# Optimization experiments

Hardware: AMD Instinct MI355X
Metric: run time of the kernel (lower is better)

## Reference

```python
import jax, jax.numpy as jnp
import numpy as np

B, N, K = 16, 1024, 20
BOX = 10.0
IN_DIM = 78
HID = 128


def setup_inputs() -> dict:
    key = jax.random.key(0)
    k1, k2, k3, k4, k5 = jax.random.split(key, 5)
    position = jax.random.uniform(k1, (B, N, 3), dtype=jnp.float32) * BOX
    # random proper orthonormal orientation matrices via QR
    R_raw = jax.random.normal(k2, (B, N, 3, 3), dtype=jnp.float32)
    orientation_R, _ = jnp.linalg.qr(R_raw)
    w1 = jax.random.normal(k3, (IN_DIM, HID), jnp.float32) * (1.0 / np.sqrt(IN_DIM))
    b1 = jnp.zeros((HID,), jnp.float32)
    w2 = jax.random.normal(k4, (HID, HID), jnp.float32) * (1.0 / np.sqrt(HID))
    b2 = jnp.zeros((HID,), jnp.float32)
    w3 = jax.random.normal(k5, (HID, 1), jnp.float32) * (1.0 / np.sqrt(HID))
    b3 = jnp.zeros((1,), jnp.float32)
    return dict(position=position, orientation_R=orientation_R,
                w1=w1, b1=b1, w2=w2, b2=b2, w3=w3, b3=b3)


def _features(position, orientation_R):
    # all-pairs displacement with minimum-image periodic boundary
    dr = position[:, :, None, :] - position[:, None, :, :]        # (B,N,N,3)
    dr = dr - BOX * jnp.round(dr / BOX)
    r2 = jnp.sum(dr * dr, axis=-1)                                # (B,N,N)
    r2 = r2 + jnp.eye(N, dtype=r2.dtype) * 1e9                    # exclude self
    neg_r2, idx = jax.lax.top_k(-r2, K)                           # (B,N,K)
    NN_R = jnp.sqrt(-neg_r2)[..., None]                           # (B,N,K,1)
    NN_dr = jnp.take_along_axis(dr, idx[..., None], axis=2)       # (B,N,K,3)
    u = NN_dr / NN_R                                              # unit separation
    inv_r = 1.0 / NN_R
    bidx = jnp.arange(B)[:, None, None]
    Rn = orientation_R[bidx, idx]                                 # (B,N,K,3,3) neighbor frames
    Rp = orientation_R                                            # (B,N,3,3) particle frame
    # pairwise dot products of principal axes: (B,N,K,3,3)
    dot = jnp.einsum('bnij,bnklj->bnkil', Rp, Rn)
    # elementwise products of every axis pair: (B,N,K,3,3,3)
    elem = Rp[:, :, None, :, None, :] * Rn[:, :, :, None, :, :]
    elem_norm = jnp.linalg.norm(elem, axis=-1)                    # (B,N,K,3,3)
    # cross products of corresponding principal axes: (B,N,K,3,3)
    cross = jnp.cross(Rp[:, :, None, :, :], Rn)
    cross_norm = jnp.linalg.norm(cross, axis=-1)                  # (B,N,K,3)
    # relative orientation R_i^T R_j: (B,N,K,3,3)
    rel = jnp.einsum('bnji,bnkjl->bnkil', Rp, Rn)
    # RBF of dr projected on principal axes
    rbf_p = jnp.exp(-jnp.einsum('bnkd,bnid->bnki', u, Rp) ** 2)   # (B,N,K,3)
    rbf_n = jnp.exp(-jnp.einsum('bnkd,bnkid->bnki', u, Rn) ** 2)  # (B,N,K,3)
    tr = rel[..., 0, 0] + rel[..., 1, 1] + rel[..., 2, 2]
    angle = jnp.arccos(jnp.clip((tr - 1.0) * 0.5, -1.0 + 1e-6, 1.0 - 1e-6))[..., None]
    feats = jnp.concatenate([
        NN_R, inv_r, u,
        dot.reshape(B, N, K, 9),
        elem.reshape(B, N, K, 27),
        elem_norm.reshape(B, N, K, 9),
        cross.reshape(B, N, K, 9),
        cross_norm,
        rel.reshape(B, N, K, 9),
        rbf_p, rbf_n, angle,
    ], axis=-1)                                                   # (B,N,K,78)
    return feats


def reference(position, orientation_R, w1, b1, w2, b2, w3, b3):
    f = _features(position, orientation_R)                        # (B,N,K,78)
    h = jnp.tanh(f @ w1 + b1)
    h = jnp.tanh(h @ w2 + b2)
    pooled = jnp.max(h, axis=2)                                   # max-pool over neighbors
    energy = pooled @ w3 + b3                                     # (B,N,1)
    return energy
```

## Files before the change

### kernel.cpp

```cpp
#include <hip/hip_runtime.h>
#include <hip/hip_bf16.h>

namespace {

constexpr int B = 16;
constexpr int N = 1024;
constexpr int K = 20;
constexpr int HID = 128;
constexpr float BOX = 10.0f;

constexpr int PPB = 4;
constexpr int MROWS = PPB * K;
constexpr int MT = 5;
constexpr int KP1 = 96;
constexpr int FP = 104;
constexpr int H1P = 136;
constexpr int SURVCAP = 96;

constexpr uint HBASE = 1872;

typedef __attribute__((ext_vector_type(8))) short short8;
typedef __attribute__((ext_vector_type(4))) float f32x4;

__device__ __forceinline__ float tanh_f(float x) {
    float e = __expf(2.0f * x);
    return 1.0f - 2.0f / (e + 1.0f);
}

__device__ __forceinline__ ushort bfb(float x) {
    __hip_bfloat16 h = __float2bfloat16(x);
    return __builtin_bit_cast(ushort, h);
}

__device__ __forceinline__ uint r2bin(uint key) {
    int bv = (int)(key >> 19) - (int)HBASE;
    return (uint)min(255, max(0, bv));
}

__device__ __forceinline__ float pbc(float d) {
    const float hi = __fsub_rn(d, BOX);
    const float lo = __fadd_rn(d, BOX);
    return d > 5.0f ? hi : (d < -5.0f ? lo : d);
}

__global__ __launch_bounds__(256) void conv_w_kernel(
    const float* __restrict__ w1, const float* __restrict__ w2,
    ushort* __restrict__ w1Th, ushort* __restrict__ w1Tl,
    ushort* __restrict__ w2Th, ushort* __restrict__ w2Tl)
{
    const int idx = blockIdx.x * 256 + threadIdx.x;
    if (idx < 128 * KP1) {
        const int n = idx / KP1, k = idx - n * KP1;
        const float v = (k < 78) ? w1[k * HID + n] : 0.0f;
        const __hip_bfloat16 h = __float2bfloat16(v);
        w1Th[idx] = __builtin_bit_cast(ushort, h);
        w1Tl[idx] = bfb(v - __bfloat162float(h));
    } else if (idx < 128 * KP1 + 128 * 128) {
        const int i = idx - 128 * KP1;
        const int n = i >> 7, k = i & 127;
        const float v = w2[k * HID + n];
        const __hip_bfloat16 h = __float2bfloat16(v);
        w2Th[i] = __builtin_bit_cast(ushort, h);
        w2Tl[i] = bfb(v - __bfloat162float(h));
    }
}

__global__ __launch_bounds__(256, 4) void fused_kernel(
    const float* __restrict__ pos, const float* __restrict__ ori,
    const float* __restrict__ b1, const float* __restrict__ b2,
    const float* __restrict__ w3, const float* __restrict__ b3,
    const ushort* __restrict__ w1Th, const ushort* __restrict__ w1Tl,
    const ushort* __restrict__ w2Th, const ushort* __restrict__ w2Tl,
    float* __restrict__ out)
{
    __shared__ __align__(16) __hip_bfloat16 fS[MROWS][FP];
    __shared__ __align__(16) ushort h1S[MROWS][H1P];
    __shared__ int   nbrS[PPB][K];
    __shared__ float RpS[PPB][9];
    __shared__ float red[4][PPB];
    __shared__ int   TS[PPB];
    __shared__ uint  scntS[PPB];

    uint* const histS = (uint*)&h1S[0][0];
    unsigned long long* const survS =
        (unsigned long long*)((char*)&h1S[0][0] + 4096);

    const int pid0 = blockIdx.x * PPB;
    const int b  = pid0 >> 10;
    const int nb = pid0 & (N - 1);
    const int t  = threadIdx.x;
    const float* posb = pos + (size_t)b * N * 3;
    const float* orib = ori + (size_t)b * N * 9;

#pragma unroll
    for (int i = 0; i < 4; ++i) histS[i * 256 + t] = 0;
    if (t < PPB) scntS[t] = 0;
    if (t < PPB * 9) RpS[t / 9][t % 9] = orib[(size_t)(nb + t / 9) * 9 + (t % 9)];

    float cx[PPB], cy[PPB], cz[PPB];
#pragma unroll
    for (int p = 0; p < PPB; ++p) {
        cx[p] = posb[(nb + p) * 3 + 0];
        cy[p] = posb[(nb + p) * 3 + 1];
        cz[p] = posb[(nb + p) * 3 + 2];
    }

    float r2v[PPB][4];
#pragma unroll
    for (int q = 0; q < 4; ++q) {
        const int j = t + q * 256;
        const float px = posb[j * 3 + 0];
        const float py = posb[j * 3 + 1];
        const float pz = posb[j * 3 + 2];
#pragma unroll
        for (int p = 0; p < PPB; ++p) {
            const float dx = pbc(__fsub_rn(cx[p], px));
            const float dy = pbc(__fsub_rn(cy[p], py));
            const float dz = pbc(__fsub_rn(cz[p], pz));
            float r2 = __fadd_rn(__fadd_rn(__fmul_rn(dx, dx), __fmul_rn(dy, dy)),
                                 __fmul_rn(dz, dz));
            if (j == nb + p) r2 = 1e9f;
            r2v[p][q] = r2;
        }
    }
    __syncthreads();

#pragma unroll
    for (int p = 0; p < PPB; ++p)
#pragma unroll
        for (int q = 0; q < 4; ++q)
            atomicAdd(&histS[p * 256 + r2bin(__float_as_uint(r2v[p][q]))], 1u);
    __syncthreads();

    {
        const int p = t >> 6, lane = t & 63;
        const uint* hp = histS + p * 256;
        const uint h0 = hp[4 * lane + 0], h1v = hp[4 * lane + 1];
        const uint h2v = hp[4 * lane + 2], h3v = hp[4 * lane + 3];
        const uint s = h0 + h1v + h2v + h3v;
        uint inc = s;
#pragma unroll
        for (int off = 1; off < 64; off <<= 1) {
            const uint v = __shfl_up(inc, off, 64);
            if (lane >= off) inc += v;
        }
        const uint exc = inc - s;
        if (exc < (uint)K && inc >= (uint)K) {
            uint c = exc; int Tb = -1;
            c += h0;  if (Tb < 0 && c >= (uint)K) Tb = 4 * lane + 0;
            c += h1v; if (Tb < 0 && c >= (uint)K) Tb = 4 * lane + 1;
            c += h2v; if (Tb < 0 && c >= (uint)K) Tb = 4 * lane + 2;
            c += h3v; if (Tb < 0 && c >= (uint)K) Tb = 4 * lane + 3;
            TS[p] = Tb;
        }
    }
    __syncthreads();

#pragma unroll
    for (int p = 0; p < PPB; ++p) {
        const uint T = (uint)TS[p];
#pragma unroll
        for (int q = 0; q < 4; ++q) {
            const uint key = __float_as_uint(r2v[p][q]);
            if (r2bin(key) <= T) {
                const uint pp = atomicAdd(&scntS[p], 1u);
                if (pp < (uint)SURVCAP)
                    survS[p * SURVCAP + pp] =
                        ((unsigned long long)key << 32) | (uint)(t + q * 256);
            }
        }
    }
    __syncthreads();

    {
        const int p = t >> 6;
        const int S = min((int)scntS[p], SURVCAP);
        const unsigned long long* sp = survS + p * SURVCAP;
#pragma unroll
        for (int half = 0; half < 2; ++half) {
            const int s = (t & 63) + half * 64;
            if (s < S) {
                const unsigned long long me = sp[s];
                int rank = 0;
                for (int jj = 0; jj < S; ++jj) rank += (sp[jj] < me) ? 1 : 0;
                if (rank < K) nbrS[p][rank] = (int)(me & 0xffffffffULL);
            }
        }
    }
    __syncthreads();

    if (t < PPB * K) {
        const int p = t / K, k = t - p * K;
        const int j = nbrS[p][k];
        float Rp[9], Rn[9];
#pragma unroll
        for (int q = 0; q < 9; ++q) Rp[q] = RpS[p][q];
#pragma unroll
        for (int q = 0; q < 9; ++q) Rn[q] = orib[(size_t)j * 9 + q];

        const float cxp = posb[(nb + p) * 3 + 0];
        const float cyp = posb[(nb + p) * 3 + 1];
        const float czp = posb[(nb + p) * 3 + 2];
        const float dx = pbc(__fsub_rn(cxp, posb[j * 3 + 0]));
        const float dy = pbc(__fsub_rn(cyp, posb[j * 3 + 1]));
        const float dz = pbc(__fsub_rn(czp, posb[j * 3 + 2]));
        const float r2 = __fadd_rn(__fadd_rn(__fmul_rn(dx, dx), __fmul_rn(dy, dy)),
                                   __fmul_rn(dz, dz));
        const float r = sqrtf(r2);
        const float invr = 1.0f / r;
        const float ux = dx * invr, uy = dy * invr, uz = dz * invr;

        __hip_bfloat16* f = fS[p * K + k];
        f[0] = __float2bfloat16(r);
        f[1] = __float2bfloat16(invr);
        f[2] = __float2bfloat16(ux);
        f[3] = __float2bfloat16(uy);
        f[4] = __float2bfloat16(uz);

        float diag[3];
#pragma unroll
        for (int i = 0; i < 3; ++i) {
#pragma unroll
            for (int l = 0; l < 3; ++l) {
                float s = 0.0f, en2 = 0.0f;
#pragma unroll
                for (int m = 0; m < 3; ++m) {
                    const float e = Rp[i * 3 + m] * Rn[l * 3 + m];
                    f[14 + i * 9 + l * 3 + m] = __float2bfloat16(e);
                    en2 += e * e;
                    s += e;
                }
                f[5 + i * 3 + l] = __float2bfloat16(s);
                f[41 + i * 3 + l] = __float2bfloat16(sqrtf(en2));
                float rr = 0.0f;
#pragma unroll
                for (int m = 0; m < 3; ++m) rr += Rp[m * 3 + i] * Rn[m * 3 + l];
                f[62 + i * 3 + l] = __float2bfloat16(rr);
                if (i == l) diag[i] = rr;
            }
        }
#pragma unroll
        for (int i = 0; i < 3; ++i) {
            const float ax = Rp[i * 3 + 0], ay = Rp[i * 3 + 1], az = Rp[i * 3 + 2];
            const float bx = Rn[i * 3 + 0], by = Rn[i * 3 + 1], bz = Rn[i * 3 + 2];
            const float ccx = ay * bz - az * by;
            const float ccy = az * bx - ax * bz;
            const float ccz = ax * by - ay * bx;
            f[50 + i * 3 + 0] = __float2bfloat16(ccx);
            f[50 + i * 3 + 1] = __float2bfloat16(ccy);
            f[50 + i * 3 + 2] = __float2bfloat16(ccz);
            f[59 + i] = __float2bfloat16(sqrtf(ccx * ccx + ccy * ccy + ccz * ccz));
            const float dp = ux * ax + uy * ay + uz * az;
            f[71 + i] = __float2bfloat16(__expf(-dp * dp));
            const float dn = ux * bx + uy * by + uz * bz;
            f[74 + i] = __float2bfloat16(__expf(-dn * dn));
        }
        const float tr = diag[0] + diag[1] + diag[2];
        float ca = (tr - 1.0f) * 0.5f;
        ca = fminf(fmaxf(ca, -1.0f + 1e-6f), 1.0f - 1e-6f);
        f[77] = __float2bfloat16(acosf(ca));
#pragma unroll
        for (int i = 78; i < KP1; ++i) f[i] = __float2bfloat16(0.0f);
    }
    __syncthreads();

    const int wv = t >> 6, ln = t & 63;
    const int lr = ln & 15, lg = ln >> 4;
    const int n0 = wv * 32 + lr, n1 = n0 + 16;

    f32x4 acc[MT][2];
    {
        const float bb0 = b1[n0], bb1 = b1[n1];
#pragma unroll
        for (int mt = 0; mt < MT; ++mt) {
            acc[mt][0] = f32x4{bb0, bb0, bb0, bb0};
            acc[mt][1] = f32x4{bb1, bb1, bb1, bb1};
        }
    }
    {
        const ushort* pb0h = w1Th + n0 * KP1 + lg * 8;
        const ushort* pb0l = w1Tl + n0 * KP1 + lg * 8;
        const ushort* pb1h = w1Th + n1 * KP1 + lg * 8;
        const ushort* pb1l = w1Tl + n1 * KP1 + lg * 8;
#pragma unroll
        for (int ks = 0; ks < 3; ++ks) {
            const short8 b0h = *reinterpret_cast<const short8*>(pb0h + ks * 32);
            const short8 b0l = *reinterpret_cast<const short8*>(pb0l + ks * 32);
            const short8 b1h = *reinterpret_cast<const short8*>(pb1h + ks * 32);
            const short8 b1l = *reinterpret_cast<const short8*>(pb1l + ks * 32);
#pragma unroll
            for (int mt = 0; mt < MT; ++mt) {
                const short8 a = *reinterpret_cast<const short8*>(
                    &fS[16 * mt + lr][ks * 32 + lg * 8]);
                acc[mt][0] = __builtin_amdgcn_mfma_f32_16x16x32_bf16(a, b0h, acc[mt][0], 0, 0, 0);
                acc[mt][0] = __builtin_amdgcn_mfma_f32_16x16x32_bf16(a, b0l, acc[mt][0], 0, 0, 0);
                acc[mt][1] = __builtin_amdgcn_mfma_f32_16x16x32_bf16(a, b1h, acc[mt][1], 0, 0, 0);
                acc[mt][1] = __builtin_amdgcn_mfma_f32_16x16x32_bf16(a, b1l, acc[mt][1], 0, 0, 0);
            }
        }
    }
#pragma unroll
    for (int mt = 0; mt < MT; ++mt)
#pragma unroll
        for (int r = 0; r < 4; ++r) {
            h1S[16 * mt + 4 * lg + r][n0] = bfb(tanh_f(acc[mt][0][r]));
            h1S[16 * mt + 4 * lg + r][n1] = bfb(tanh_f(acc[mt][1][r]));
        }
    __syncthreads();

    {
        const float bb0 = b2[n0], bb1 = b2[n1];
#pragma unroll
        for (int mt = 0; mt < MT; ++mt) {
            acc[mt][0] = f32x4{bb0, bb0, bb0, bb0};
            acc[mt][1] = f32x4{bb1, bb1, bb1, bb1};
        }
    }
    {
        const ushort* pb0h = w2Th + n0 * HID + lg * 8;
        const ushort* pb0l = w2Tl + n0 * HID + lg * 8;
        const ushort* pb1h = w2Th + n1 * HID + lg * 8;
        const ushort* pb1l = w2Tl + n1 * HID + lg * 8;
#pragma unroll
        for (int ks = 0; ks < 4; ++ks) {
            const short8 b0h = *reinterpret_cast<const short8*>(pb0h + ks * 32);
            const short8 b0l = *reinterpret_cast<const short8*>(pb0l + ks * 32);
            const short8 b1h = *reinterpret_cast<const short8*>(pb1h + ks * 32);
            const short8 b1l = *reinterpret_cast<const short8*>(pb1l + ks * 32);
#pragma unroll
            for (int mt = 0; mt < MT; ++mt) {
                const short8 a = *reinterpret_cast<const short8*>(
                    &h1S[16 * mt + lr][ks * 32 + lg * 8]);
                acc[mt][0] = __builtin_amdgcn_mfma_f32_16x16x32_bf16(a, b0h, acc[mt][0], 0, 0, 0);
                acc[mt][0] = __builtin_amdgcn_mfma_f32_16x16x32_bf16(a, b0l, acc[mt][0], 0, 0, 0);
                acc[mt][1] = __builtin_amdgcn_mfma_f32_16x16x32_bf16(a, b1h, acc[mt][1], 0, 0, 0);
                acc[mt][1] = __builtin_amdgcn_mfma_f32_16x16x32_bf16(a, b1l, acc[mt][1], 0, 0, 0);
            }
        }
    }

#pragma unroll
    for (int mt = 0; mt < MT; ++mt)
#pragma unroll
        for (int nt = 0; nt < 2; ++nt)
#pragma unroll
            for (int r = 0; r < 4; ++r) acc[mt][nt][r] = tanh_f(acc[mt][nt][r]);

    const float w3n0 = w3[n0], w3n1 = w3[n1];
#pragma unroll
    for (int p = 0; p < PPB; ++p) {
        float m0 = -3.0e38f, m1 = -3.0e38f;
#pragma unroll
        for (int mt = 0; mt < MT; ++mt) {
            const bool in = (uint)(4 * mt + lg - 5 * p) < 5u;
#pragma unroll
            for (int r = 0; r < 4; ++r) {
                m0 = fmaxf(m0, in ? acc[mt][0][r] : -3.0e38f);
                m1 = fmaxf(m1, in ? acc[mt][1][r] : -3.0e38f);
            }
        }
        m0 = fmaxf(m0, __shfl_xor(m0, 16, 64));
        m0 = fmaxf(m0, __shfl_xor(m0, 32, 64));
        m1 = fmaxf(m1, __shfl_xor(m1, 16, 64));
        m1 = fmaxf(m1, __shfl_xor(m1, 32, 64));
        float v = m0 * w3n0 + m1 * w3n1;
#pragma unroll
        for (int off = 1; off < 16; off <<= 1) v += __shfl_xor(v, off, 64);
        if (ln == 0) red[wv][p] = v;
    }
    __syncthreads();
    if (t < PPB) out[pid0 + t] = red[0][t] + red[1][t] + red[2][t] + red[3][t] + b3[0];
}

}

extern "C" void kernel_launch(void* const* d_in, const int* in_sizes, int n_in,
                              void* d_out, int out_size, void* d_ws, size_t ws_size,
                              hipStream_t stream) {
    const float* pos = (const float*)d_in[0];
    const float* ori = (const float*)d_in[1];
    const float* w1  = (const float*)d_in[2];
    const float* b1  = (const float*)d_in[3];
    const float* w2  = (const float*)d_in[4];
    const float* b2  = (const float*)d_in[5];
    const float* w3  = (const float*)d_in[6];
    const float* b3  = (const float*)d_in[7];
    float* out = (float*)d_out;

    ushort* w1Th = (ushort*)d_ws;
    ushort* w1Tl = w1Th + 128 * 96;
    ushort* w2Th = w1Tl + 128 * 96;
    ushort* w2Tl = w2Th + 128 * 128;

    const int convElems = 128 * 96 + 128 * 128;
    conv_w_kernel<<<dim3((convElems + 255) / 256), dim3(256), 0, stream>>>(
        w1, w2, w1Th, w1Tl, w2Th, w2Tl);
    fused_kernel<<<dim3(B * N / PPB), dim3(256), 0, stream>>>(
        pos, ori, b1, b2, w3, b3, w1Th, w1Tl, w2Th, w2Tl, out);
}
```

Before: 170.4 us.

## Split neighbor selection into its own kernel and merge weight conversion into it

Moves the histogram/top-K neighbor selection out of the fused MLP kernel into a separate select kernel with launch bounds allowing 8 blocks per CU. The selected indices go to workspace as 16-bit values. The weight bf16 hi/lo conversion now runs as extra blocks of that same launch. The aim is to stop the selection phase's register and LDS needs from limiting the MLP kernel's occupancy, and to drop one launch. The cost is a global round trip for the neighbor indices and a kernel boundary between the two phases.

Result: no change. 167.9 us (-1.5%).

```diff
diff --git a/kernel.cpp b/kernel.cpp
--- a/kernel.cpp
+++ b/kernel.cpp
@@ -19,6 +19,10 @@
 
 constexpr uint HBASE = 1872;
 
+constexpr int GRID_SEL  = B * N / PPB;
+constexpr int CONV_ELEMS = 128 * KP1 + 128 * 128;
+constexpr int GRID_CONV = (CONV_ELEMS + 255) / 256;
+
 typedef __attribute__((ext_vector_type(8))) short short8;
 typedef __attribute__((ext_vector_type(4))) float f32x4;
 
@@ -43,59 +47,47 @@
     return d > 5.0f ? hi : (d < -5.0f ? lo : d);
 }
 
-__global__ __launch_bounds__(256) void conv_w_kernel(
+__global__ __launch_bounds__(256, 8) void select_kernel(
+    const float* __restrict__ pos,
     const float* __restrict__ w1, const float* __restrict__ w2,
     ushort* __restrict__ w1Th, ushort* __restrict__ w1Tl,
-    ushort* __restrict__ w2Th, ushort* __restrict__ w2Tl)
+    ushort* __restrict__ w2Th, ushort* __restrict__ w2Tl,
+    ushort* __restrict__ nbr)
 {
-    const int idx = blockIdx.x * 256 + threadIdx.x;
-    if (idx < 128 * KP1) {
-        const int n = idx / KP1, k = idx - n * KP1;
-        const float v = (k < 78) ? w1[k * HID + n] : 0.0f;
-        const __hip_bfloat16 h = __float2bfloat16(v);
-        w1Th[idx] = __builtin_bit_cast(ushort, h);
-        w1Tl[idx] = bfb(v - __bfloat162float(h));
-    } else if (idx < 128 * KP1 + 128 * 128) {
-        const int i = idx - 128 * KP1;
-        const int n = i >> 7, k = i & 127;
-        const float v = w2[k * HID + n];
-        const __hip_bfloat16 h = __float2bfloat16(v);
-        w2Th[i] = __builtin_bit_cast(ushort, h);
-        w2Tl[i] = bfb(v - __bfloat162float(h));
-    }
-}
-
-__global__ __launch_bounds__(256, 4) void fused_kernel(
-    const float* __restrict__ pos, const float* __restrict__ ori,
-    const float* __restrict__ b1, const float* __restrict__ b2,
-    const float* __restrict__ w3, const float* __restrict__ b3,
-    const ushort* __restrict__ w1Th, const ushort* __restrict__ w1Tl,
-    const ushort* __restrict__ w2Th, const ushort* __restrict__ w2Tl,
-    float* __restrict__ out)
-{
-    __shared__ __align__(16) __hip_bfloat16 fS[MROWS][FP];
-    __shared__ __align__(16) ushort h1S[MROWS][H1P];
-    __shared__ int   nbrS[PPB][K];
-    __shared__ float RpS[PPB][9];
-    __shared__ float red[4][PPB];
-    __shared__ int   TS[PPB];
-    __shared__ uint  scntS[PPB];
-
-    uint* const histS = (uint*)&h1S[0][0];
-    unsigned long long* const survS =
-        (unsigned long long*)((char*)&h1S[0][0] + 4096);
+    const int t = threadIdx.x;
+
+    if (blockIdx.x >= GRID_SEL) {
+        const int idx = (blockIdx.x - GRID_SEL) * 256 + t;
+        if (idx < 128 * KP1) {
+            const int n = idx / KP1, k = idx - n * KP1;
+            const float v = (k < 78) ? w1[k * HID + n] : 0.0f;
+            const __hip_bfloat16 h = __float2bfloat16(v);
+            w1Th[idx] = __builtin_bit_cast(ushort, h);
+            w1Tl[idx] = bfb(v - __bfloat162float(h));
+        } else if (idx < CONV_ELEMS) {
+            const int i = idx - 128 * KP1;
+            const int n = i >> 7, k = i & 127;
+            const float v = w2[k * HID + n];
+            const __hip_bfloat16 h = __float2bfloat16(v);
+            w2Th[i] = __builtin_bit_cast(ushort, h);
+            w2Tl[i] = bfb(v - __bfloat162float(h));
+        }
+        return;
+    }
+
+    __shared__ uint histS[PPB][256];
+    __shared__ unsigned long long survS[PPB][SURVCAP];
+    __shared__ int  TS[PPB];
+    __shared__ uint scntS[PPB];
 
     const int pid0 = blockIdx.x * PPB;
     const int b  = pid0 >> 10;
     const int nb = pid0 & (N - 1);
-    const int t  = threadIdx.x;
     const float* posb = pos + (size_t)b * N * 3;
-    const float* orib = ori + (size_t)b * N * 9;
-
-#pragma unroll
-    for (int i = 0; i < 4; ++i) histS[i * 256 + t] = 0;
+
+#pragma unroll
+    for (int p = 0; p < PPB; ++p) histS[p][t] = 0;
     if (t < PPB) scntS[t] = 0;
-    if (t < PPB * 9) RpS[t / 9][t % 9] = orib[(size_t)(nb + t / 9) * 9 + (t % 9)];
 
     float cx[PPB], cy[PPB], cz[PPB];
 #pragma unroll
@@ -129,14 +121,13 @@
     for (int p = 0; p < PPB; ++p)
 #pragma unroll
         for (int q = 0; q < 4; ++q)
-            atomicAdd(&histS[p * 256 + r2bin(__float_as_uint(r2v[p][q]))], 1u);
+            atomicAdd(&histS[p][r2bin(__float_as_uint(r2v[p][q]))], 1u);
     __syncthreads();
 
     {
         const int p = t >> 6, lane = t & 63;
-        const uint* hp = histS + p * 256;
-        const uint h0 = hp[4 * lane + 0], h1v = hp[4 * lane + 1];
-        const uint h2v = hp[4 * lane + 2], h3v = hp[4 * lane + 3];
+        const uint h0 = histS[p][4 * lane + 0], h1v = histS[p][4 * lane + 1];
+        const uint h2v = histS[p][4 * lane + 2], h3v = histS[p][4 * lane + 3];
         const uint s = h0 + h1v + h2v + h3v;
         uint inc = s;
 #pragma unroll
@@ -165,7 +156,7 @@
             if (r2bin(key) <= T) {
                 const uint pp = atomicAdd(&scntS[p], 1u);
                 if (pp < (uint)SURVCAP)
-                    survS[p * SURVCAP + pp] =
+                    survS[p][pp] =
                         ((unsigned long long)key << 32) | (uint)(t + q * 256);
             }
         }
@@ -175,23 +166,46 @@
     {
         const int p = t >> 6;
         const int S = min((int)scntS[p], SURVCAP);
-        const unsigned long long* sp = survS + p * SURVCAP;
 #pragma unroll
         for (int half = 0; half < 2; ++half) {
             const int s = (t & 63) + half * 64;
             if (s < S) {
-                const unsigned long long me = sp[s];
+                const unsigned long long me = survS[p][s];
                 int rank = 0;
-                for (int jj = 0; jj < S; ++jj) rank += (sp[jj] < me) ? 1 : 0;
-                if (rank < K) nbrS[p][rank] = (int)(me & 0xffffffffULL);
-            }
-        }
-    }
+                for (int jj = 0; jj < S; ++jj) rank += (survS[p][jj] < me) ? 1 : 0;
+                if (rank < K)
+                    nbr[(size_t)(pid0 + p) * K + rank] = (ushort)(me & 0xffffULL);
+            }
+        }
+    }
+}
+
+__global__ __launch_bounds__(256, 4) void mlp_kernel(
+    const float* __restrict__ pos, const float* __restrict__ ori,
+    const float* __restrict__ b1, const float* __restrict__ b2,
+    const float* __restrict__ w3, const float* __restrict__ b3,
+    const ushort* __restrict__ w1Th, const ushort* __restrict__ w1Tl,
+    const ushort* __restrict__ w2Th, const ushort* __restrict__ w2Tl,
+    const ushort* __restrict__ nbr, float* __restrict__ out)
+{
+    __shared__ __align__(16) __hip_bfloat16 fS[MROWS][FP];
+    __shared__ __align__(16) ushort h1S[MROWS][H1P];
+    __shared__ float RpS[PPB][9];
+    __shared__ float red[4][PPB];
+
+    const int pid0 = blockIdx.x * PPB;
+    const int b  = pid0 >> 10;
+    const int nb = pid0 & (N - 1);
+    const int t  = threadIdx.x;
+    const float* posb = pos + (size_t)b * N * 3;
+    const float* orib = ori + (size_t)b * N * 9;
+
+    if (t < PPB * 9) RpS[t / 9][t % 9] = orib[(size_t)(nb + t / 9) * 9 + (t % 9)];
     __syncthreads();
 
     if (t < PPB * K) {
         const int p = t / K, k = t - p * K;
-        const int j = nbrS[p][k];
+        const int j = (int)nbr[(size_t)(pid0 + p) * K + k];
         float Rp[9], Rn[9];
 #pragma unroll
         for (int q = 0; q < 9; ++q) Rp[q] = RpS[p][q];
@@ -388,13 +402,13 @@
     float* out = (float*)d_out;
 
     ushort* w1Th = (ushort*)d_ws;
-    ushort* w1Tl = w1Th + 128 * 96;
-    ushort* w2Th = w1Tl + 128 * 96;
+    ushort* w1Tl = w1Th + 128 * KP1;
+    ushort* w2Th = w1Tl + 128 * KP1;
     ushort* w2Tl = w2Th + 128 * 128;
-
-    const int convElems = 128 * 96 + 128 * 128;
-    conv_w_kernel<<<dim3((convElems + 255) / 256), dim3(256), 0, stream>>>(
-        w1, w2, w1Th, w1Tl, w2Th, w2Tl);
-    fused_kernel<<<dim3(B * N / PPB), dim3(256), 0, stream>>>(
-        pos, ori, b1, b2, w3, b3, w1Th, w1Tl, w2Th, w2Tl, out);
-}
+    ushort* nbr  = w2Tl + 128 * 128;
+
+    select_kernel<<<dim3(GRID_SEL + GRID_CONV), dim3(256), 0, stream>>>(
+        pos, w1, w2, w1Th, w1Tl, w2Th, w2Tl, nbr);
+    mlp_kernel<<<dim3(GRID_SEL), dim3(256), 0, stream>>>(
+        pos, ori, b1, b2, w3, b3, w1Th, w1Tl, w2Th, w2Tl, nbr, out);
+}
```
